# Optimization experiments

Measured on AMD Instinct MI355X. Metric: run time of the kernel, lower is better.

The kernel has to match this reference:

```python
import jax, jax.numpy as jnp
import numpy as np

D_MODEL, D_STATE, EXPAND = 1024, 16, 2
D_INNER = D_MODEL * EXPAND
BATCH, SEQ = 4, 2048
DT = 0.1

def setup_inputs() -> dict:
    key = jax.random.key(0)
    ks = jax.random.split(key, 12)
    s = 0.02
    inp = {
        "x": jax.random.normal(ks[0], (BATCH, SEQ, D_MODEL), jnp.float32),
        "B_mod": jax.random.normal(ks[1], (BATCH, D_STATE), jnp.float32) * 0.1,
        "C_mod": jax.random.normal(ks[2], (BATCH, D_STATE), jnp.float32) * 0.1,
        "W_in": jax.random.normal(ks[3], (D_MODEL, 2 * D_INNER), jnp.float32) * s,
        "b_in": jnp.zeros((2 * D_INNER,), jnp.float32),
        "conv_w": jax.random.normal(ks[4], (D_INNER, 1, 3), jnp.float32) * 0.3,
        "conv_b": jnp.zeros((D_INNER,), jnp.float32),
        "A_log": jnp.tile(jnp.log(jnp.arange(1, D_STATE + 1, dtype=jnp.float32))[None, :], (D_INNER, 1)),
        "D": jnp.ones((D_INNER,), jnp.float32),
        "W_B": jax.random.normal(ks[5], (D_INNER, D_STATE), jnp.float32) * s,
        "b_B": jnp.zeros((D_STATE,), jnp.float32),
        "W_C": jax.random.normal(ks[6], (D_INNER, D_STATE), jnp.float32) * s,
        "b_C": jnp.zeros((D_STATE,), jnp.float32),
        "W_out": jax.random.normal(ks[7], (D_INNER, D_MODEL), jnp.float32) * s,
        "b_out": jnp.zeros((D_MODEL,), jnp.float32),
    }
    return inp

def _silu(v):
    return v * jax.nn.sigmoid(v)

def reference(x, B_mod, C_mod, W_in, b_in, conv_w, conv_b, A_log, D, W_B, b_B, W_C, b_C, W_out, b_out):
    # in_proj + split + gate
    xr = x @ W_in + b_in                      # (B, L, 2*D_INNER)
    x_ssm, x_res = jnp.split(xr, 2, axis=-1)
    x_ssm = _silu(x_ssm)
    # depthwise conv1d, kernel 3, padding 1
    xc = jnp.transpose(x_ssm, (0, 2, 1))      # (B, C, L)
    xc = jax.lax.conv_general_dilated(
        xc, conv_w, window_strides=(1,), padding=[(1, 1)],
        dimension_numbers=("NCH", "OIH", "NCH"), feature_group_count=D_INNER)
    xc = xc + conv_b[None, :, None]
    x_ssm = jnp.transpose(xc, (0, 2, 1))      # (B, L, D_INNER)
    # SSM params
    A = -jnp.exp(A_log)                       # (D_INNER, D_STATE)
    A_bar = jnp.exp(A * DT)
    B = x_ssm @ W_B + b_B + B_mod[:, None, :] # (B, L, D_STATE)
    C = x_ssm @ W_C + b_C + C_mod[:, None, :]
    # sequential scan over time
    def step(h, inp):
        xt, Bt, Ct = inp                      # (B,D_INNER), (B,S), (B,S)
        h = A_bar[None] * h + xt[:, :, None] * Bt[:, None, :]
        yt = jnp.einsum("bds,bs->bd", h, Ct)
        return h, yt
    h0 = jnp.zeros((x.shape[0], D_INNER, D_STATE), x.dtype)
    xs = (jnp.moveaxis(x_ssm, 1, 0), jnp.moveaxis(B, 1, 0), jnp.moveaxis(C, 1, 0))
    _, ys = jax.lax.scan(step, h0, xs)        # (L, B, D_INNER)
    y = jnp.moveaxis(ys, 0, 1) + D[None, None, :] * x_ssm
    y = y * _silu(x_res)
    return y @ W_out + b_out
```

## Files before the change

### kernel.cpp

```cpp
#include <hip/hip_runtime.h>
#include <stdint.h>

#define D_MODEL 1024
#define D_STATE 16
#define D_INNER 2048
#define BATCH   4
#define SEQ     2048
#define ML      (BATCH*SEQ)
#define CH      64
#define NCHUNK  (SEQ/CH)
#define KSEG    8

typedef unsigned short u16;
typedef u16   u16x8  __attribute__((ext_vector_type(8)));
typedef short s16x8  __attribute__((ext_vector_type(8)));
typedef float f32x4  __attribute__((ext_vector_type(4)));

__device__ __forceinline__ float b2f(u16 u){
  union { uint32_t i; float f; } v; v.i = ((uint32_t)u) << 16; return v.f;
}
__device__ __forceinline__ u16 f2b(float f){
  uint32_t x = __float_as_uint(f);
  return (u16)((x + 0x7fffu + ((x >> 16) & 1u)) >> 16);
}
__device__ __forceinline__ float silu_f(float v){
  return v / (1.f + __expf(-v));
}
__device__ __forceinline__ void gl_lds16(const void* gp, void* lp){
  __builtin_amdgcn_global_load_lds(
      (const __attribute__((address_space(1))) void*)gp,
      (__attribute__((address_space(3))) void*)lp, 16, 0, 0);
}

__global__ __launch_bounds__(256) void transpose_cast_k(const float* __restrict__ in,
                                                        u16* __restrict__ out,
                                                        int R, int C){
  __shared__ float tile[32][33];
  int bx = blockIdx.x * 32, by = blockIdx.y * 32;
  int tx = threadIdx.x & 31, ty = threadIdx.x >> 5;
  #pragma unroll
  for (int i = 0; i < 32; i += 8)
    tile[ty + i][tx] = in[(size_t)(by + ty + i) * C + bx + tx];
  __syncthreads();
  #pragma unroll
  for (int i = 0; i < 32; i += 8)
    out[(size_t)(bx + ty + i) * R + by + tx] = f2b(tile[tx][ty + i]);
}

__global__ __launch_bounds__(256) void cast_k(const float* __restrict__ in,
                                              u16* __restrict__ out){
  size_t i = ((size_t)blockIdx.x * 256 + threadIdx.x) * 8;
  f32x4 a = *(const f32x4*)(in + i);
  f32x4 b = *(const f32x4*)(in + i + 4);
  u16x8 o;
  #pragma unroll
  for (int j = 0; j < 4; ++j){ o[j] = f2b(a[j]); o[4+j] = f2b(b[j]); }
  *(u16x8*)(out + i) = o;
}

__global__ __launch_bounds__(256) void bc_wt_k(const float* __restrict__ W_B,
                                               const float* __restrict__ W_C,
                                               u16* __restrict__ Wt){
  int n = blockIdx.y;
  int k = blockIdx.x * 256 + threadIdx.x;
  const float* src = (n < 16) ? W_B : W_C;
  Wt[(size_t)n * D_INNER + k] = f2b(src[(size_t)k * 16 + (n & 15)]);
}

#define G1_K  1024
#define G1_NT (G1_K/64)

__global__ __launch_bounds__(512, 2) void gemm1_k(const u16* __restrict__ A,
                                                  const u16* __restrict__ Bt,
                                                  const float* __restrict__ bias,
                                                  u16* __restrict__ out0,
                                                  u16* __restrict__ out1){
  __shared__ __align__(16) u16 ldsA[4*8192];
  __shared__ __align__(16) u16 ldsB[4*8192];

  const int bid = blockIdx.x;
  const int xcd = bid & 7, t2 = bid >> 3;
  const int n0 = (xcd*2 + (t2 & 1)) * 256;
  const int m0 = (t2 >> 1) * 256;

  const int tid  = threadIdx.x;
  const int wave = tid >> 6, lane = tid & 63;
  const int wr = wave >> 2;
  const int wc = wave & 3;
  const int lrow = lane & 15;
  const int q    = lane >> 4;
  const int colu = ((q ^ ((lrow >> 1) & 3)) << 3);
  const int srow8   = lane >> 3;
  const int schunk8 = (((lane & 7) ^ ((lane >> 4) & 3)) << 3);

  auto stageA = [&](int buf, int h, int k0){
    const u16* s0 = A + (size_t)(m0 + h*128 + wave*16 + srow8) * G1_K + (k0 + schunk8);
    u16* d = ldsA + (buf*2 + h)*8192 + wave*16*64;
    gl_lds16(s0, d);
    gl_lds16(s0 + (size_t)8*G1_K, d + 8*64);
  };
  auto stageB = [&](int buf, int h, int k0){
    const u16* s0 = Bt + (size_t)(n0 + h*128 + wave*16 + srow8) * G1_K + (k0 + schunk8);
    u16* d = ldsB + (buf*2 + h)*8192 + wave*16*64;
    gl_lds16(s0, d);
    gl_lds16(s0 + (size_t)8*G1_K, d + 8*64);
  };

  f32x4 acc[8][4];
  #pragma unroll
  for (int i = 0; i < 8; ++i)
    #pragma unroll
    for (int j = 0; j < 4; ++j) acc[i][j] = (f32x4){0.f,0.f,0.f,0.f};
  s16x8 af[8][2], bfr[4][2];

  stageA(0,0,0); stageB(0,0,0); stageB(0,1,0); stageA(0,1,0);
  asm volatile("s_waitcnt vmcnt(4)" ::: "memory");
  stageB(1,0,64); stageB(1,1,64); stageA(1,0,64);
  asm volatile("s_waitcnt vmcnt(6)" ::: "memory");
  __builtin_amdgcn_s_barrier();

  auto mfma_pair = [&](int mi){
    #pragma unroll
    for (int nj = 0; nj < 4; ++nj) {
      #pragma unroll
      for (int kk = 0; kk < 2; ++kk) {
        acc[mi][nj]   = __builtin_amdgcn_mfma_f32_16x16x32_bf16(af[mi][kk],   bfr[nj][kk], acc[mi][nj],   0,0,0);
        acc[mi+1][nj] = __builtin_amdgcn_mfma_f32_16x16x32_bf16(af[mi+1][kk], bfr[nj][kk], acc[mi+1][nj], 0,0,0);
      }
    }
  };

  #pragma unroll 2
  for (int tt = 0; tt < G1_NT; ++tt) {
    const int buf = tt & 1;
    const u16* Ab = ldsA + (buf*2 + wr)*8192 + lrow*64 + colu;
    const u16* Bb = ldsB + (buf*2 + (wc >> 1))*8192 + ((wc & 1)*64 + lrow)*64 + colu;
    const int k1 = (tt+1 < G1_NT ? tt+1 : G1_NT-1) * 64;
    const int k2 = (tt+2 < G1_NT ? tt+2 : G1_NT-1) * 64;

    #pragma unroll
    for (int nj = 0; nj < 4; ++nj){
      bfr[nj][0] = *(const s16x8*)(Bb + nj*16*64);
      bfr[nj][1] = *(const s16x8*)(Bb + nj*16*64 + 32);
    }
    af[0][0] = *(const s16x8*)(Ab);
    af[0][1] = *(const s16x8*)(Ab + 32);
    af[1][0] = *(const s16x8*)(Ab + 16*64);
    af[1][1] = *(const s16x8*)(Ab + 16*64 + 32);
    stageA(buf ^ 1, 1, k1);
    __builtin_amdgcn_s_barrier();
    __builtin_amdgcn_s_setprio(1);
    mfma_pair(0);
    __builtin_amdgcn_s_setprio(0);
    __builtin_amdgcn_s_barrier();

    #pragma unroll
    for (int i = 2; i < 5; ++i){
      af[i][0] = *(const s16x8*)(Ab + i*16*64);
      af[i][1] = *(const s16x8*)(Ab + i*16*64 + 32);
    }
    stageB(buf, 0, k2);
    __builtin_amdgcn_s_barrier();
    __builtin_amdgcn_s_setprio(1);
    mfma_pair(2);
    __builtin_amdgcn_s_setprio(0);
    __builtin_amdgcn_s_barrier();

    #pragma unroll
    for (int i = 5; i < 8; ++i){
      af[i][0] = *(const s16x8*)(Ab + i*16*64);
      af[i][1] = *(const s16x8*)(Ab + i*16*64 + 32);
    }
    stageB(buf, 1, k2);
    __builtin_amdgcn_s_barrier();
    __builtin_amdgcn_s_setprio(1);
    mfma_pair(4);
    __builtin_amdgcn_s_setprio(0);
    __builtin_amdgcn_s_barrier();

    stageA(buf, 0, k2);
    asm volatile("s_waitcnt vmcnt(6)" ::: "memory");
    __builtin_amdgcn_s_barrier();
    __builtin_amdgcn_s_setprio(1);
    mfma_pair(6);
    __builtin_amdgcn_s_setprio(0);
    __builtin_amdgcn_s_barrier();
  }
  asm volatile("s_waitcnt vmcnt(0)" ::: "memory");

  #pragma unroll
  for (int nj = 0; nj < 4; ++nj) {
    const int col = n0 + wc*64 + nj*16 + lrow;
    const float bv = bias[col];
    u16* op = (col < D_INNER) ? (out0 + col) : (out1 + (col - D_INNER));
    #pragma unroll
    for (int mi = 0; mi < 8; ++mi) {
      #pragma unroll
      for (int r = 0; r < 4; ++r) {
        const int row = m0 + wr*128 + mi*16 + q*4 + r;
        op[(size_t)row * D_INNER] = f2b(silu_f(acc[mi][nj][r] + bv));
      }
    }
  }
}

template<int MODE>
__global__ __launch_bounds__(256) void gemm_bt(const u16* __restrict__ A,
                                               const u16* __restrict__ Bt,
                                               const float* __restrict__ bias,
                                               u16* __restrict__ out0,
                                               u16* __restrict__ out1,
                                               float* __restrict__ outf,
                                               int M, int N, int K, int n_per_xcd){
  __shared__ __align__(16) u16 Asb[2][128*32];
  __shared__ __align__(16) u16 Bsb[2][128*32];
  const int bid = blockIdx.x;
  const int xcd = bid & 7, t2 = bid >> 3;
  const int n0 = (xcd * n_per_xcd + (t2 % n_per_xcd)) * 128;
  const int m0 = (t2 / n_per_xcd) * 128;
  const int t    = threadIdx.x;
  const int wave = t >> 6, lane = t & 63;
  const int wm   = (wave >> 1) * 64, wn = (wave & 1) * 64;
  const int lrow = lane & 15, kq = (lane >> 4) * 8;
  const int srow = lane >> 2;
  const int scol = (lane & 3) * 8;

  f32x4 acc[4][4];
  #pragma unroll
  for (int i = 0; i < 4; ++i)
    #pragma unroll
    for (int j = 0; j < 4; ++j)
      acc[i][j] = (f32x4){0.f, 0.f, 0.f, 0.f};

  auto stage = [&](int buf, int k0){
    #pragma unroll
    for (int i = 0; i < 2; ++i) {
      int R0 = (wave*2 + i) * 16;
      gl_lds16(&A [(size_t)(m0 + R0 + srow)*K + k0 + scol], &Asb[buf][R0*32]);
      gl_lds16(&Bt[(size_t)(n0 + R0 + srow)*K + k0 + scol], &Bsb[buf][R0*32]);
    }
  };

  const int KT = K >> 5;
  stage(0, 0);
  __syncthreads();
  for (int kt = 0; kt < KT; ++kt) {
    const int cur = kt & 1;
    if (kt + 1 < KT) stage(1 - cur, (kt + 1) * 32);
    s16x8 af[4], bfr[4];
    #pragma unroll
    for (int i = 0; i < 4; ++i) af[i]  = *(const s16x8*)&Asb[cur][(wm + i*16 + lrow)*32 + kq];
    #pragma unroll
    for (int j = 0; j < 4; ++j) bfr[j] = *(const s16x8*)&Bsb[cur][(wn + j*16 + lrow)*32 + kq];
    #pragma unroll
    for (int i = 0; i < 4; ++i)
      #pragma unroll
      for (int j = 0; j < 4; ++j)
        acc[i][j] = __builtin_amdgcn_mfma_f32_16x16x32_bf16(af[i], bfr[j], acc[i][j], 0, 0, 0);
    __syncthreads();
  }

  const int Nh = N >> 1;
  #pragma unroll
  for (int i = 0; i < 4; ++i) {
    #pragma unroll
    for (int j = 0; j < 4; ++j) {
      int col = n0 + wn + j*16 + lrow;
      float bv = bias[col];
      #pragma unroll
      for (int r = 0; r < 4; ++r) {
        int row = m0 + wm + i*16 + (lane >> 4)*4 + r;
        float v = acc[i][j][r] + bv;
        if (MODE == 0) {
          outf[(size_t)row * N + col] = v;
        } else {
          float s = silu_f(v);
          if (col < Nh) out0[(size_t)row * Nh + col]        = f2b(s);
          else          out1[(size_t)row * Nh + (col - Nh)] = f2b(s);
        }
      }
    }
  }
}

__global__ __launch_bounds__(256) void conv_k(const u16* __restrict__ xs,
    const float* __restrict__ conv_w, const float* __restrict__ conv_b,
    u16* __restrict__ xconv){
  int bl = blockIdx.x;
  int l = bl & (SEQ-1);
  int d = threadIdx.x * 8;
  const u16* row0 = xs + (size_t)bl * D_INNER + d;

  float f0[8], fm[8], fp[8];
  { u16x8 v = *(const u16x8*)row0;
    #pragma unroll
    for (int j = 0; j < 8; ++j) f0[j] = b2f(v[j]); }
  if (l > 0) {
    u16x8 v = *(const u16x8*)(row0 - D_INNER);
    #pragma unroll
    for (int j = 0; j < 8; ++j) fm[j] = b2f(v[j]);
  } else {
    #pragma unroll
    for (int j = 0; j < 8; ++j) fm[j] = 0.f;
  }
  if (l < SEQ-1) {
    u16x8 v = *(const u16x8*)(row0 + D_INNER);
    #pragma unroll
    for (int j = 0; j < 8; ++j) fp[j] = b2f(v[j]);
  } else {
    #pragma unroll
    for (int j = 0; j < 8; ++j) fp[j] = 0.f;
  }

  const float* wp = conv_w + (size_t)d * 3;
  float wl[24];
  #pragma unroll
  for (int q = 0; q < 6; ++q){
    f32x4 v = *(const f32x4*)(wp + q*4);
    #pragma unroll
    for (int j = 0; j < 4; ++j) wl[q*4 + j] = v[j];
  }
  float cb[8];
  { f32x4 c0 = *(const f32x4*)(conv_b + d), c1 = *(const f32x4*)(conv_b + d + 4);
    #pragma unroll
    for (int j = 0; j < 4; ++j){ cb[j] = c0[j]; cb[4+j] = c1[j]; } }

  u16x8 o;
  #pragma unroll
  for (int j = 0; j < 8; ++j)
    o[j] = f2b(wl[3*j]*fm[j] + wl[3*j+1]*f0[j] + wl[3*j+2]*fp[j] + cb[j]);
  *(u16x8*)(xconv + (size_t)bl * D_INNER + d) = o;
}

__global__ __launch_bounds__(256) void bc_gemm_k(const u16* __restrict__ xconv,
                                                 const u16* __restrict__ Wt,
                                                 float* __restrict__ partial){
  __shared__ __align__(16) u16 Asb[128*40];
  __shared__ __align__(16) u16 Wsb[32*40];
  const int kseg = blockIdx.x;
  const int m0   = blockIdx.y * 128;
  const int t    = threadIdx.x;
  const int wave = t >> 6, lane = t & 63;
  const int wm   = wave * 32;
  const int lrow = lane & 15, kq = (lane >> 4) * 8;

  f32x4 acc[2][2];
  #pragma unroll
  for (int i = 0; i < 2; ++i)
    #pragma unroll
    for (int j = 0; j < 2; ++j)
      acc[i][j] = (f32x4){0.f, 0.f, 0.f, 0.f};

  const int kbase = kseg * (D_INNER / KSEG);
  for (int ks = 0; ks < (D_INNER / KSEG); ks += 32) {
    int k0 = kbase + ks;
    #pragma unroll
    for (int i = 0; i < 2; ++i) {
      int f = (i*256 + t) * 8;
      int r = f >> 5, c = f & 31;
      *(u16x8*)&Asb[r*40 + c] = *(const u16x8*)&xconv[(size_t)(m0 + r)*D_INNER + k0 + c];
    }
    if (t < 128) {
      int f = t * 8;
      int r = f >> 5, c = f & 31;
      *(u16x8*)&Wsb[r*40 + c] = *(const u16x8*)&Wt[(size_t)r*D_INNER + k0 + c];
    }
    __syncthreads();
    s16x8 af[2], wf[2];
    #pragma unroll
    for (int i = 0; i < 2; ++i) af[i] = *(const s16x8*)&Asb[(wm + i*16 + lrow)*40 + kq];
    #pragma unroll
    for (int j = 0; j < 2; ++j) wf[j] = *(const s16x8*)&Wsb[(j*16 + lrow)*40 + kq];
    #pragma unroll
    for (int i = 0; i < 2; ++i)
      #pragma unroll
      for (int j = 0; j < 2; ++j)
        acc[i][j] = __builtin_amdgcn_mfma_f32_16x16x32_bf16(af[i], wf[j], acc[i][j], 0, 0, 0);
    __syncthreads();
  }

  #pragma unroll
  for (int i = 0; i < 2; ++i)
    #pragma unroll
    for (int j = 0; j < 2; ++j)
      #pragma unroll
      for (int r = 0; r < 4; ++r) {
        int row = m0 + wm + i*16 + (lane >> 4)*4 + r;
        int col = j*16 + lrow;
        partial[((size_t)kseg * ML + row) * 32 + col] = acc[i][j][r];
      }
}

__global__ __launch_bounds__(256) void bc_reduce_k(const float* __restrict__ partial,
    const float* __restrict__ b_B, const float* __restrict__ B_mod,
    const float* __restrict__ b_C, const float* __restrict__ C_mod,
    float* __restrict__ Bbuf, float* __restrict__ Cbuf){
  int g = blockIdx.x * 256 + threadIdx.x;
  int row = g >> 5, col = g & 31;
  int b = row >> 11;
  float s = 0.f;
  #pragma unroll
  for (int seg = 0; seg < KSEG; ++seg)
    s += partial[(size_t)seg * ML * 32 + g];
  if (col < 16) Bbuf[(size_t)row*16 + col]      = s + b_B[col]      + B_mod[b*16 + col];
  else          Cbuf[(size_t)row*16 + col - 16] = s + b_C[col - 16] + C_mod[b*16 + col - 16];
}

__global__ __launch_bounds__(256) void state_k(const u16* __restrict__ xconv,
    const float* __restrict__ Bbuf, const float* __restrict__ A_log,
    float* __restrict__ hend){
  int c = blockIdx.x, db = blockIdx.y, b = blockIdx.z;
  int d = db*256 + threadIdx.x;

  float Abar[16];
  #pragma unroll
  for (int s = 0; s < 16; ++s)
    Abar[s] = __expf(-0.1f * __expf(A_log[d*16 + s]));
  float h[16];
  #pragma unroll
  for (int s = 0; s < 16; ++s) h[s] = 0.f;

  size_t base = (size_t)b * SEQ * D_INNER + (size_t)c * CH * D_INNER + d;
  const float* Br = Bbuf + ((size_t)b * SEQ + (size_t)c * CH) * 16;

  float Bc[16];
  #pragma unroll
  for (int s = 0; s < 16; ++s) Bc[s] = Br[s];
  float xn = b2f(xconv[base]);

  for (int l = 0; l < CH; ++l){
    float x = xn;
    float Bl[16];
    #pragma unroll
    for (int s = 0; s < 16; ++s) Bl[s] = Bc[s];
    if (l < CH-1){
      xn = b2f(xconv[base + (size_t)(l+1)*D_INNER]);
      #pragma unroll
      for (int s = 0; s < 16; ++s) Bc[s] = Br[(l+1)*16 + s];
    }
    #pragma unroll
    for (int s = 0; s < 16; ++s)
      h[s] = Abar[s]*h[s] + x*Bl[s];
  }
  float* hp = hend + (((size_t)(b*NCHUNK + c))*D_INNER + d)*16;
  #pragma unroll
  for (int q = 0; q < 4; ++q)
    *(f32x4*)(hp + q*4) = (f32x4){h[q*4], h[q*4+1], h[q*4+2], h[q*4+3]};
}

__global__ __launch_bounds__(256) void prefix_k(const float* __restrict__ hend,
    const float* __restrict__ A_log, float* __restrict__ hin){
  int g = blockIdx.x*256 + threadIdx.x;
  int s = g & 15;
  int d = (g >> 4) & (D_INNER-1);
  int b = g >> 15;
  float decay = __expf(-0.1f * (float)CH * __expf(A_log[d*16 + s]));
  size_t stride = (size_t)D_INNER * 16;
  const float* he = hend + (size_t)b*NCHUNK*stride + (size_t)d*16 + s;
  float*       hi = hin  + (size_t)b*NCHUNK*stride + (size_t)d*16 + s;
  float h = 0.f;
  for (int c0 = 0; c0 < NCHUNK; c0 += 8){
    float v[8];
    #pragma unroll
    for (int i = 0; i < 8; ++i) v[i] = he[(size_t)(c0+i)*stride];
    #pragma unroll
    for (int i = 0; i < 8; ++i){
      hi[(size_t)(c0+i)*stride] = h;
      h = decay*h + v[i];
    }
  }
}

__global__ __launch_bounds__(256) void scan2_k(const u16* __restrict__ xconv,
    const u16* __restrict__ gate, const float* __restrict__ Bbuf, const float* __restrict__ Cbuf,
    const float* __restrict__ A_log, const float* __restrict__ Dp,
    const float* __restrict__ hin, u16* __restrict__ ybuf){
  int c = blockIdx.x, db = blockIdx.y, b = blockIdx.z;
  int d = db*256 + threadIdx.x;

  float Abar[16];
  #pragma unroll
  for (int s = 0; s < 16; ++s)
    Abar[s] = __expf(-0.1f * __expf(A_log[d*16 + s]));
  float h[16];
  const float* hp = hin + (((size_t)(b*NCHUNK + c))*D_INNER + d)*16;
  #pragma unroll
  for (int q = 0; q < 4; ++q){
    f32x4 v = *(const f32x4*)(hp + q*4);
    #pragma unroll
    for (int j = 0; j < 4; ++j) h[q*4 + j] = v[j];
  }
  float Dd = Dp[d];

  size_t base = (size_t)b * SEQ * D_INNER + (size_t)c * CH * D_INNER + d;
  const float* Br = Bbuf + ((size_t)b * SEQ + (size_t)c * CH) * 16;
  const float* Cr = Cbuf + ((size_t)b * SEQ + (size_t)c * CH) * 16;

  float Bc[16], Cc[16];
  #pragma unroll
  for (int s = 0; s < 16; ++s){ Bc[s] = Br[s]; Cc[s] = Cr[s]; }
  float xn = b2f(xconv[base]);
  float gn = b2f(gate[base]);

  for (int l = 0; l < CH; ++l){
    float x = xn, g = gn;
    float Bl[16], Cl[16];
    #pragma unroll
    for (int s = 0; s < 16; ++s){ Bl[s] = Bc[s]; Cl[s] = Cc[s]; }
    if (l < CH-1){
      size_t idx = base + (size_t)(l+1)*D_INNER;
      xn = b2f(xconv[idx]); gn = b2f(gate[idx]);
      #pragma unroll
      for (int s = 0; s < 16; ++s){ Bc[s] = Br[(l+1)*16 + s]; Cc[s] = Cr[(l+1)*16 + s]; }
    }
    float ya[4] = {0.f, 0.f, 0.f, 0.f};
    #pragma unroll
    for (int s = 0; s < 16; ++s){
      float hv = Abar[s]*h[s] + x*Bl[s];
      h[s] = hv;
      ya[s & 3] += hv * Cl[s];
    }
    float y = ((ya[0]+ya[1]) + (ya[2]+ya[3]) + Dd*x) * g;
    ybuf[base + (size_t)l*D_INNER] = f2b(y);
  }
}

extern "C" void kernel_launch(void* const* d_in, const int* in_sizes, int n_in,
                              void* d_out, int out_size, void* d_ws, size_t ws_size,
                              hipStream_t stream){
  const float* x      = (const float*)d_in[0];
  const float* B_mod  = (const float*)d_in[1];
  const float* C_mod  = (const float*)d_in[2];
  const float* W_in   = (const float*)d_in[3];
  const float* b_in   = (const float*)d_in[4];
  const float* conv_w = (const float*)d_in[5];
  const float* conv_b = (const float*)d_in[6];
  const float* A_log  = (const float*)d_in[7];
  const float* Dp     = (const float*)d_in[8];
  const float* W_B    = (const float*)d_in[9];
  const float* b_B    = (const float*)d_in[10];
  const float* W_C    = (const float*)d_in[11];
  const float* b_C    = (const float*)d_in[12];
  const float* W_out  = (const float*)d_in[13];
  const float* b_out  = (const float*)d_in[14];
  float* out = (float*)d_out;

  char* ws = (char*)d_ws;
  size_t off = 0;
  auto alloc = [&](size_t bytes)->char* {
    char* p = ws + off; off += (bytes + 255) & ~(size_t)255; return p;
  };
  u16* Wt_in  = (u16*)alloc((size_t)(2*D_INNER)*D_MODEL*2);
  u16* Wt_out = (u16*)alloc((size_t)D_MODEL*D_INNER*2);
  u16* xs     = (u16*)alloc((size_t)ML*D_INNER*2);
  u16* gatep  = (u16*)alloc((size_t)ML*D_INNER*2);
  u16* xconv  = (u16*)alloc((size_t)ML*D_INNER*2);
  float* Bbuf = (float*)alloc((size_t)ML*D_STATE*4);
  float* Cbuf = (float*)alloc((size_t)ML*D_STATE*4);
  u16* xbf    = (u16*)alloc((size_t)ML*D_MODEL*2);
  float* hin  = (float*)alloc((size_t)BATCH*NCHUNK*D_INNER*16*4);
  u16* Wt_bc  = (u16*)alloc((size_t)32*D_INNER*2);
  float* hend    = (float*)xbf;
  float* partial = (float*)Wt_in;
  u16* ybuf = xs;

  transpose_cast_k<<<dim3((2*D_INNER)/32, D_MODEL/32), 256, 0, stream>>>(W_in, Wt_in, D_MODEL, 2*D_INNER);
  transpose_cast_k<<<dim3(D_MODEL/32, D_INNER/32),     256, 0, stream>>>(W_out, Wt_out, D_INNER, D_MODEL);
  cast_k<<<dim3((ML*D_MODEL)/(256*8)), 256, 0, stream>>>(x, xbf);
  bc_wt_k<<<dim3(D_INNER/256, 32), 256, 0, stream>>>(W_B, W_C, Wt_bc);

  gemm1_k<<<dim3(512), 512, 0, stream>>>(xbf, Wt_in, b_in, xs, gatep);

  conv_k<<<dim3(ML), 256, 0, stream>>>(xs, conv_w, conv_b, xconv);

  bc_gemm_k<<<dim3(KSEG, ML/128), 256, 0, stream>>>(xconv, Wt_bc, partial);
  bc_reduce_k<<<dim3((ML*32)/256), 256, 0, stream>>>(
      partial, b_B, B_mod, b_C, C_mod, Bbuf, Cbuf);

  state_k<<<dim3(NCHUNK, D_INNER/256, BATCH), 256, 0, stream>>>(xconv, Bbuf, A_log, hend);
  prefix_k<<<dim3((BATCH*D_INNER*16)/256), 256, 0, stream>>>(hend, A_log, hin);
  scan2_k<<<dim3(NCHUNK, D_INNER/256, BATCH), 256, 0, stream>>>(
      xconv, gatep, Bbuf, Cbuf, A_log, Dp, hin, ybuf);

  gemm_bt<0><<<dim3(512), 256, 0, stream>>>(
      ybuf, Wt_out, b_out, nullptr, nullptr, out, ML, D_MODEL, D_INNER, 1);
}
```

Baseline: 368.8 us.

## Restructure in-proj GEMM pipeline with fragment-major LDS layout and staged epilogue

Changes the LDS staging layout of the in-projection GEMM to a fragment-ordered layout, so reads become lane-contiguous without XOR swizzling. The main loop is rewritten to double-buffer B fragments across tiles and prefetch the next tile's A/B fragments during the last MFMA quarter, with explicit lgkmcnt waits and sched barriers. The epilogue now stages the bf16 output tile through a padded LDS buffer and writes 16-byte coalesced rows instead of scattered 2-byte stores. It relies on hand-tuned wait counts and a larger shared allocation, which could reduce occupancy or introduce hazards if the counts are wrong.

```diff
diff --git a/kernel.cpp b/kernel.cpp
--- a/kernel.cpp
+++ b/kernel.cpp
@@ -75,8 +75,9 @@
                                                   const float* __restrict__ bias,
                                                   u16* __restrict__ out0,
                                                   u16* __restrict__ out1){
-  __shared__ __align__(16) u16 ldsA[4*8192];
-  __shared__ __align__(16) u16 ldsB[4*8192];
+  __shared__ __align__(16) u16 ldsAll[256*264];
+  u16* ldsA = ldsAll;
+  u16* ldsB = ldsAll + 4*8192;
 
   const int bid = blockIdx.x;
   const int xcd = bid & 7, t2 = bid >> 3;
@@ -89,119 +90,146 @@
   const int wc = wave & 3;
   const int lrow = lane & 15;
   const int q    = lane >> 4;
-  const int colu = ((q ^ ((lrow >> 1) & 3)) << 3);
-  const int srow8   = lane >> 3;
-  const int schunk8 = (((lane & 7) ^ ((lane >> 4) & 3)) << 3);
 
   auto stageA = [&](int buf, int h, int k0){
-    const u16* s0 = A + (size_t)(m0 + h*128 + wave*16 + srow8) * G1_K + (k0 + schunk8);
-    u16* d = ldsA + (buf*2 + h)*8192 + wave*16*64;
-    gl_lds16(s0, d);
-    gl_lds16(s0 + (size_t)8*G1_K, d + 8*64);
+    const u16* s = A + (size_t)(m0 + h*128 + wave*16 + lrow) * G1_K + k0 + q*8;
+    u16* d = ldsA + (buf*2 + h)*8192 + wave*1024;
+    gl_lds16(s,      d);
+    gl_lds16(s + 32, d + 512);
   };
   auto stageB = [&](int buf, int h, int k0){
-    const u16* s0 = Bt + (size_t)(n0 + h*128 + wave*16 + srow8) * G1_K + (k0 + schunk8);
-    u16* d = ldsB + (buf*2 + h)*8192 + wave*16*64;
-    gl_lds16(s0, d);
-    gl_lds16(s0 + (size_t)8*G1_K, d + 8*64);
+    const u16* s = Bt + (size_t)(n0 + h*128 + wave*16 + lrow) * G1_K + k0 + q*8;
+    u16* d = ldsB + (buf*2 + h)*8192 + wave*1024;
+    gl_lds16(s,      d);
+    gl_lds16(s + 32, d + 512);
   };
 
+  const u16* aRd0 = ldsA + wr*8192 + (size_t)lane*8;
+  const u16* bRd0 = ldsB + (wc>>1)*8192 + (wc&1)*4096 + (size_t)lane*8;
+
   f32x4 acc[8][4];
   #pragma unroll
   for (int i = 0; i < 8; ++i)
     #pragma unroll
     for (int j = 0; j < 4; ++j) acc[i][j] = (f32x4){0.f,0.f,0.f,0.f};
-  s16x8 af[8][2], bfr[4][2];
-
-  stageA(0,0,0); stageB(0,0,0); stageB(0,1,0); stageA(0,1,0);
+
+  s16x8 aA[2][2], aB[2][2];
+  s16x8 bX[4][2], bY[4][2];
+
+  #define READ_AQ(dst, Q, nb)                                            \
+    { const u16* p_ = aRd0 + (nb)*16384 + (Q)*2048;                      \
+      dst[0][0] = *(const s16x8*)(p_);                                   \
+      dst[0][1] = *(const s16x8*)(p_ + 512);                             \
+      dst[1][0] = *(const s16x8*)(p_ + 1024);                            \
+      dst[1][1] = *(const s16x8*)(p_ + 1536); }
+  #define READ_B8(dst, nb)                                               \
+    { const u16* p_ = bRd0 + (nb)*16384;                                 \
+      _Pragma("unroll")                                                  \
+      for (int nj_ = 0; nj_ < 4; ++nj_){                                 \
+        dst[nj_][0] = *(const s16x8*)(p_ + nj_*1024);                    \
+        dst[nj_][1] = *(const s16x8*)(p_ + nj_*1024 + 512); } }
+  #define MFMA_Q(Q, AF, BF)                                              \
+    { _Pragma("unroll")                                                  \
+      for (int nj_ = 0; nj_ < 4; ++nj_){                                 \
+        _Pragma("unroll")                                                \
+        for (int kk_ = 0; kk_ < 2; ++kk_){                               \
+          acc[2*(Q)][nj_]   = __builtin_amdgcn_mfma_f32_16x16x32_bf16(AF[0][kk_], BF[nj_][kk_], acc[2*(Q)][nj_],   0,0,0); \
+          acc[2*(Q)+1][nj_] = __builtin_amdgcn_mfma_f32_16x16x32_bf16(AF[1][kk_], BF[nj_][kk_], acc[2*(Q)+1][nj_], 0,0,0); } } }
+
+  stageA(0,0,0); stageA(0,1,0); stageB(0,0,0); stageB(0,1,0);
+  stageB(1,0,64); stageB(1,1,64);
   asm volatile("s_waitcnt vmcnt(4)" ::: "memory");
-  stageB(1,0,64); stageB(1,1,64); stageA(1,0,64);
-  asm volatile("s_waitcnt vmcnt(6)" ::: "memory");
   __builtin_amdgcn_s_barrier();
-
-  auto mfma_pair = [&](int mi){
-    #pragma unroll
-    for (int nj = 0; nj < 4; ++nj) {
-      #pragma unroll
-      for (int kk = 0; kk < 2; ++kk) {
-        acc[mi][nj]   = __builtin_amdgcn_mfma_f32_16x16x32_bf16(af[mi][kk],   bfr[nj][kk], acc[mi][nj],   0,0,0);
-        acc[mi+1][nj] = __builtin_amdgcn_mfma_f32_16x16x32_bf16(af[mi+1][kk], bfr[nj][kk], acc[mi+1][nj], 0,0,0);
-      }
-    }
-  };
-
-  #pragma unroll 2
-  for (int tt = 0; tt < G1_NT; ++tt) {
-    const int buf = tt & 1;
-    const u16* Ab = ldsA + (buf*2 + wr)*8192 + lrow*64 + colu;
-    const u16* Bb = ldsB + (buf*2 + (wc >> 1))*8192 + ((wc & 1)*64 + lrow)*64 + colu;
+  __builtin_amdgcn_sched_barrier(0);
+  READ_B8(bX, 0);
+  READ_AQ(aA, 0, 0);
+
+  auto tile_body = [&](int tt, int buf, s16x8 (&bC)[4][2], s16x8 (&bN)[4][2]){
     const int k1 = (tt+1 < G1_NT ? tt+1 : G1_NT-1) * 64;
     const int k2 = (tt+2 < G1_NT ? tt+2 : G1_NT-1) * 64;
-
-    #pragma unroll
-    for (int nj = 0; nj < 4; ++nj){
-      bfr[nj][0] = *(const s16x8*)(Bb + nj*16*64);
-      bfr[nj][1] = *(const s16x8*)(Bb + nj*16*64 + 32);
-    }
-    af[0][0] = *(const s16x8*)(Ab);
-    af[0][1] = *(const s16x8*)(Ab + 32);
-    af[1][0] = *(const s16x8*)(Ab + 16*64);
-    af[1][1] = *(const s16x8*)(Ab + 16*64 + 32);
-    stageA(buf ^ 1, 1, k1);
-    __builtin_amdgcn_s_barrier();
+    const int nb = buf ^ 1;
+
+    READ_AQ(aB, 1, buf);
+    stageA(nb, 1, k1);
+    stageA(nb, 0, k1);
+    __builtin_amdgcn_s_barrier();
+    asm volatile("s_waitcnt lgkmcnt(4)" ::: "memory");
+    __builtin_amdgcn_sched_barrier(0);
     __builtin_amdgcn_s_setprio(1);
-    mfma_pair(0);
+    MFMA_Q(0, aA, bC);
     __builtin_amdgcn_s_setprio(0);
     __builtin_amdgcn_s_barrier();
 
-    #pragma unroll
-    for (int i = 2; i < 5; ++i){
-      af[i][0] = *(const s16x8*)(Ab + i*16*64);
-      af[i][1] = *(const s16x8*)(Ab + i*16*64 + 32);
-    }
+    READ_AQ(aA, 2, buf);
     stageB(buf, 0, k2);
     __builtin_amdgcn_s_barrier();
+    asm volatile("s_waitcnt lgkmcnt(4)" ::: "memory");
+    __builtin_amdgcn_sched_barrier(0);
     __builtin_amdgcn_s_setprio(1);
-    mfma_pair(2);
+    MFMA_Q(1, aB, bC);
     __builtin_amdgcn_s_setprio(0);
     __builtin_amdgcn_s_barrier();
 
-    #pragma unroll
-    for (int i = 5; i < 8; ++i){
-      af[i][0] = *(const s16x8*)(Ab + i*16*64);
-      af[i][1] = *(const s16x8*)(Ab + i*16*64 + 32);
-    }
+    READ_AQ(aB, 3, buf);
     stageB(buf, 1, k2);
     __builtin_amdgcn_s_barrier();
+    asm volatile("s_waitcnt lgkmcnt(4)" ::: "memory");
+    __builtin_amdgcn_sched_barrier(0);
     __builtin_amdgcn_s_setprio(1);
-    mfma_pair(4);
+    MFMA_Q(2, aA, bC);
     __builtin_amdgcn_s_setprio(0);
     __builtin_amdgcn_s_barrier();
 
-    stageA(buf, 0, k2);
-    asm volatile("s_waitcnt vmcnt(6)" ::: "memory");
-    __builtin_amdgcn_s_barrier();
+    asm volatile("s_waitcnt vmcnt(4)" ::: "memory");
+    __builtin_amdgcn_s_barrier();
+    __builtin_amdgcn_sched_barrier(0);
+    READ_B8(bN, nb);
+    READ_AQ(aA, 0, nb);
+    asm volatile("s_waitcnt lgkmcnt(12)" ::: "memory");
+    __builtin_amdgcn_sched_barrier(0);
     __builtin_amdgcn_s_setprio(1);
-    mfma_pair(6);
+    MFMA_Q(3, aB, bC);
     __builtin_amdgcn_s_setprio(0);
     __builtin_amdgcn_s_barrier();
-  }
+  };
+
+  for (int tt2 = 0; tt2 < G1_NT; tt2 += 2) {
+    tile_body(tt2,     0, bX, bY);
+    tile_body(tt2 + 1, 1, bY, bX);
+  }
+
   asm volatile("s_waitcnt vmcnt(0)" ::: "memory");
+  __syncthreads();
 
   #pragma unroll
   for (int nj = 0; nj < 4; ++nj) {
-    const int col = n0 + wc*64 + nj*16 + lrow;
-    const float bv = bias[col];
-    u16* op = (col < D_INNER) ? (out0 + col) : (out1 + (col - D_INNER));
+    const int colg = n0 + wc*64 + nj*16 + lrow;
+    const float bv = bias[colg];
+    const int coll = wc*64 + nj*16 + lrow;
     #pragma unroll
     for (int mi = 0; mi < 8; ++mi) {
       #pragma unroll
       for (int r = 0; r < 4; ++r) {
-        const int row = m0 + wr*128 + mi*16 + q*4 + r;
-        op[(size_t)row * D_INNER] = f2b(silu_f(acc[mi][nj][r] + bv));
+        const int rowl = wr*128 + mi*16 + q*4 + r;
+        ldsAll[rowl*264 + coll] = f2b(silu_f(acc[mi][nj][r] + bv));
       }
     }
   }
+  __syncthreads();
+
+  u16* op = (n0 < D_INNER) ? out0 : out1;
+  const int colbase = n0 & (D_INNER - 1);
+  #pragma unroll
+  for (int it = 0; it < 16; ++it) {
+    const int f   = it*512 + tid;
+    const int row = f >> 5;
+    const int ch  = f & 31;
+    u16x8 v = *(const u16x8*)(ldsAll + row*264 + ch*8);
+    *(u16x8*)(op + (size_t)(m0 + row)*D_INNER + colbase + ch*8) = v;
+  }
+  #undef READ_AQ
+  #undef READ_B8
+  #undef MFMA_Q
 }
 
 template<int MODE>
```

Result: no change. 372.4 us (+1.0%).
